# Kernel tuning notes

Measured on AMD Instinct MI355X. Metric: run time of the kernel, lower is better.

The kernel has to match this reference:

```python
import jax, jax.numpy as jnp
import numpy as np

LN_EPS = 1e-5
NEG_INF = -1e30


def setup_inputs() -> dict:
    key = jax.random.key(0)
    k1, k2, k3 = jax.random.split(key, 3)
    B, N, D = 8192, 64, 64
    fi = jax.random.normal(k1, (B, N, D), dtype=jnp.float32)
    # orthogonal-init correlation matrix (matches nn.init.orthogonal_)
    a = jax.random.normal(k2, (D, D), dtype=jnp.float32)
    q, r = jnp.linalg.qr(a)
    correlation_mat = q * jnp.sign(jnp.diag(r))[None, :]
    ln1_gamma = jnp.ones((D,), dtype=jnp.float32)
    ln1_beta = jnp.zeros((D,), dtype=jnp.float32)
    last_w = jax.random.normal(k3, (1, 2 * D), dtype=jnp.float32) * 0.05
    last_b = jnp.zeros((1,), dtype=jnp.float32)
    return {"fi": fi, "correlation_mat": correlation_mat,
            "ln1_gamma": ln1_gamma, "ln1_beta": ln1_beta,
            "last_w": last_w, "last_b": last_b}


def _layer_norm(x, gamma, beta):
    mu = jnp.mean(x, axis=-1, keepdims=True)
    var = jnp.mean(jnp.square(x - mu), axis=-1, keepdims=True)
    return (x - mu) * jax.lax.rsqrt(var + LN_EPS) * gamma + beta


def reference(fi, correlation_mat, ln1_gamma, ln1_beta, last_w, last_b):
    B, N, D = fi.shape
    # pairwise bilinear scores: beta[b,i,j] = fi[b,i] @ C @ fi[b,j]
    fiC = jnp.einsum('bid,de->bie', fi, correlation_mat)        # [B,N,D]
    beta = jnp.einsum('bie,bje->bij', fiC, fi)                  # [B,N,N]
    # exclude self (i==j), matching the Python loop which skips j==i
    diag_mask = jnp.eye(N, dtype=bool)
    beta = jnp.where(diag_mask[None, :, :], NEG_INF, beta)
    alpha = jax.nn.softmax(beta, axis=-1)                       # [B,N,N]
    vi = jnp.einsum('bij,bjd->bid', alpha, fi)                  # [B,N,D]
    vi = jax.nn.relu(_layer_norm(vi, ln1_gamma, ln1_beta))
    all_inputs = jnp.concatenate([fi, vi], axis=-1)             # [B,N,2D]
    weight = jax.nn.sigmoid(jnp.einsum('bnk,ok->bno', all_inputs, last_w) + last_b)
    return weight  # [B, N, 1]
```

## Files before the change

kernel.cpp:

```cpp
#include <hip/hip_runtime.h>
#include <hip/hip_bf16.h>

typedef __attribute__((ext_vector_type(8))) short short8;
typedef __attribute__((ext_vector_type(4))) float floatx4;

constexpr float LN_EPS = 1e-5f;
constexpr float NEG_INF_V = -1e30f;

__device__ __forceinline__ unsigned short bf16hi_sw(float x) {
    unsigned int u = __builtin_bit_cast(unsigned int, x);
    u += 0x7FFFu + ((u >> 16) & 1u);
    return (unsigned short)(u >> 16);
}
__device__ __forceinline__ float bf16f(unsigned short h) {
    unsigned int u = ((unsigned int)h) << 16;
    return __builtin_bit_cast(float, u);
}
__device__ __forceinline__ unsigned int pk2(float a, float b) {
    float2 f2; f2.x = a; f2.y = b;
    __hip_bfloat162 h2 = __float22bfloat162_rn(f2);
    unsigned int u;
    __builtin_memcpy(&u, &h2, sizeof(u));
    return u;
}
__device__ __forceinline__ void splitpk(float a, float b,
                                        unsigned int& H, unsigned int& L) {
    H = pk2(a, b);
    const float ha = __builtin_bit_cast(float, H << 16);
    const float hb = __builtin_bit_cast(float, H & 0xFFFF0000u);
    L = pk2(a - ha, b - hb);
}

__device__ __forceinline__ unsigned int permlo(unsigned int A, unsigned int B) {
    return __builtin_amdgcn_perm(B, A, 0x05040100u);
}
__device__ __forceinline__ unsigned int permhi(unsigned int A, unsigned int B) {
    return __builtin_amdgcn_perm(B, A, 0x07060302u);
}

template<int CTRL>
__device__ __forceinline__ float dppadd(float v) {
    int t = __builtin_amdgcn_update_dpp(0, __builtin_bit_cast(int, v),
                                        CTRL, 0xF, 0xF, true);
    return v + __builtin_bit_cast(float, t);
}
template<int CTRL>
__device__ __forceinline__ float dppmax(float v) {
    int t = __builtin_amdgcn_update_dpp(0, __builtin_bit_cast(int, v),
                                        CTRL, 0xF, 0xF, true);
    return fmaxf(v, __builtin_bit_cast(float, t));
}
__device__ __forceinline__ float rsum16(float v) {
    v = dppadd<0x121>(v); v = dppadd<0x122>(v);
    v = dppadd<0x124>(v); v = dppadd<0x128>(v);
    return v;
}
__device__ __forceinline__ float rmax16(float v) {
    v = dppmax<0x121>(v); v = dppmax<0x122>(v);
    v = dppmax<0x124>(v); v = dppmax<0x128>(v);
    return v;
}

__device__ __forceinline__ int eoff(int r, int c) {
    return r * 64 + ((((c >> 3) ^ r) & 7) << 3) + (c & 7);
}
__device__ __forceinline__ int goff(int r, int g) {
    return r * 64 + (((g ^ r) & 7) << 3);
}

__global__ void prep_corr(const float* __restrict__ corr,
                          unsigned short* __restrict__ ws) {
    const int tid  = threadIdx.x;
    const int lane = tid & 63;
    const int t    = tid >> 6;
    const int nn   = lane & 15;
    const int q    = lane >> 4;
    const int brow = 16 * t + nn;
    #pragma unroll
    for (int kk = 0; kk < 2; ++kk) {
        const int kbase = (kk * 4 + q) * 8;
        short8 H8, L8;
        #pragma unroll
        for (int e = 0; e < 8; ++e) {
            const float v = corr[(kbase + e) * 64 + brow];
            const unsigned short hh = bf16hi_sw(v);
            const unsigned short ll = bf16hi_sw(v - bf16f(hh));
            H8[e] = (short)hh;
            L8[e] = (short)ll;
        }
        const int idx = ((t * 2 + kk) * 64 + lane) * 8;
        *(short8*)&ws[idx]        = H8;
        *(short8*)&ws[4096 + idx] = L8;
    }
}

template<bool USEWS>
__global__ __launch_bounds__(256, 4)
void attn_mfma(const float* __restrict__ fi,
               const float* __restrict__ corr,
               const unsigned short* __restrict__ wsC,
               const float* __restrict__ ln_g,
               const float* __restrict__ ln_b,
               const float* __restrict__ lw,
               const float* __restrict__ lb,
               float* __restrict__ out)
{
    __shared__ __align__(16) unsigned short sFiH[4096], sFiL[4096];
    __shared__ __align__(16) unsigned short sFtH[4096];
    __shared__ __align__(16) unsigned short sPH[4096], sPL[4096];

    const int tid  = threadIdx.x;
    const int lane = tid & 63;
    const int w    = tid >> 6;
    const int n    = lane & 15;
    const int quad = lane >> 4;
    const size_t blk = blockIdx.x;

    const short8* wCH = (const short8*)wsC;
    const short8* wCL = (const short8*)(wsC + 4096);

    const int C = 4 * n;
    const int R = 4 * (tid >> 4);
    float d0v[4];
    {
        const float* fb = fi + blk * 4096;
        float4 v[4];
        #pragma unroll
        for (int i = 0; i < 4; ++i)
            v[i] = *(const float4*)(fb + (R + i) * 64 + C);

        const float4 w0v = *(const float4*)&lw[C];
        #pragma unroll
        for (int i = 0; i < 4; ++i) {
            float p = v[i].x * w0v.x + v[i].y * w0v.y
                    + v[i].z * w0v.z + v[i].w * w0v.w;
            d0v[i] = rsum16(p);
        }

        unsigned int H01[4], H23[4], L01[4], L23[4];
        #pragma unroll
        for (int i = 0; i < 4; ++i) {
            splitpk(v[i].x, v[i].y, H01[i], L01[i]);
            splitpk(v[i].z, v[i].w, H23[i], L23[i]);
        }
        #pragma unroll
        for (int i = 0; i < 4; ++i) {
            uint2 H = {H01[i], H23[i]};
            uint2 L = {L01[i], L23[i]};
            *(uint2*)&sFiH[eoff(R + i, C)] = H;
            *(uint2*)&sFiL[eoff(R + i, C)] = L;
        }
        uint2 t0 = {permlo(H01[0], H01[1]), permlo(H01[2], H01[3])};
        uint2 t1 = {permhi(H01[0], H01[1]), permhi(H01[2], H01[3])};
        uint2 t2 = {permlo(H23[0], H23[1]), permlo(H23[2], H23[3])};
        uint2 t3 = {permhi(H23[0], H23[1]), permhi(H23[2], H23[3])};
        *(uint2*)&sFtH[eoff(C + 0, R)] = t0;
        *(uint2*)&sFtH[eoff(C + 1, R)] = t1;
        *(uint2*)&sFtH[eoff(C + 2, R)] = t2;
        *(uint2*)&sFtH[eoff(C + 3, R)] = t3;
    }

    if constexpr (!USEWS) {
        float4 cv[4];
        #pragma unroll
        for (int i = 0; i < 4; ++i)
            cv[i] = *(const float4*)(corr + (size_t)(R + i) * 64 + C);
        unsigned int cH01[4], cH23[4], cL01[4], cL23[4];
        #pragma unroll
        for (int i = 0; i < 4; ++i) {
            splitpk(cv[i].x, cv[i].y, cH01[i], cL01[i]);
            splitpk(cv[i].z, cv[i].w, cH23[i], cL23[i]);
        }
        uint2 h0 = {permlo(cH01[0], cH01[1]), permlo(cH01[2], cH01[3])};
        uint2 h1 = {permhi(cH01[0], cH01[1]), permhi(cH01[2], cH01[3])};
        uint2 h2 = {permlo(cH23[0], cH23[1]), permlo(cH23[2], cH23[3])};
        uint2 h3 = {permhi(cH23[0], cH23[1]), permhi(cH23[2], cH23[3])};
        uint2 l0 = {permlo(cL01[0], cL01[1]), permlo(cL01[2], cL01[3])};
        uint2 l1 = {permhi(cL01[0], cL01[1]), permhi(cL01[2], cL01[3])};
        uint2 l2 = {permlo(cL23[0], cL23[1]), permlo(cL23[2], cL23[3])};
        uint2 l3 = {permhi(cL23[0], cL23[1]), permhi(cL23[2], cL23[3])};
        *(uint2*)&sPH[eoff(C + 0, R)] = h0;  *(uint2*)&sPL[eoff(C + 0, R)] = l0;
        *(uint2*)&sPH[eoff(C + 1, R)] = h1;  *(uint2*)&sPL[eoff(C + 1, R)] = l1;
        *(uint2*)&sPH[eoff(C + 2, R)] = h2;  *(uint2*)&sPL[eoff(C + 2, R)] = l2;
        *(uint2*)&sPH[eoff(C + 3, R)] = h3;  *(uint2*)&sPL[eoff(C + 3, R)] = l3;
        __syncthreads();
    }

    const int arow = 16 * w + n;

    short8 Ah[2], Al[2];
    #pragma unroll
    for (int kk = 0; kk < 2; ++kk) {
        Ah[kk] = *(const short8*)&sFiH[goff(arow, kk * 4 + quad)];
        Al[kk] = *(const short8*)&sFiL[goff(arow, kk * 4 + quad)];
    }
    floatx4 acc1[4];
    #pragma unroll
    for (int t = 0; t < 4; ++t) {
        floatx4 acc = {0.f, 0.f, 0.f, 0.f};
        #pragma unroll
        for (int kk = 0; kk < 2; ++kk) {
            short8 bh, bl;
            if constexpr (USEWS) {
                const int f = t * 2 + kk;
                bh = wCH[f * 64 + lane];
                bl = wCL[f * 64 + lane];
            } else {
                const int brow = 16 * t + n;
                bh = *(const short8*)&sPH[goff(brow, kk * 4 + quad)];
                bl = *(const short8*)&sPL[goff(brow, kk * 4 + quad)];
            }
            acc = __builtin_amdgcn_mfma_f32_16x16x32_bf16(Ah[kk], bh, acc, 0, 0, 0);
            acc = __builtin_amdgcn_mfma_f32_16x16x32_bf16(Al[kk], bh, acc, 0, 0, 0);
            acc = __builtin_amdgcn_mfma_f32_16x16x32_bf16(Ah[kk], bl, acc, 0, 0, 0);
        }
        acc1[t] = acc;
    }

    if constexpr (!USEWS) __syncthreads();

    #pragma unroll
    for (int t = 0; t < 4; ++t) {
        const int col = 16 * t + n;
        const int row = 16 * w + quad * 4;
        unsigned int H01, L01, H23, L23;
        splitpk(acc1[t][0], acc1[t][1], H01, L01);
        splitpk(acc1[t][2], acc1[t][3], H23, L23);
        sPH[eoff(row + 0, col)] = (unsigned short)H01;
        sPH[eoff(row + 1, col)] = (unsigned short)(H01 >> 16);
        sPH[eoff(row + 2, col)] = (unsigned short)H23;
        sPH[eoff(row + 3, col)] = (unsigned short)(H23 >> 16);
        sPL[eoff(row + 0, col)] = (unsigned short)L01;
        sPL[eoff(row + 1, col)] = (unsigned short)(L01 >> 16);
        sPL[eoff(row + 2, col)] = (unsigned short)L23;
        sPL[eoff(row + 3, col)] = (unsigned short)(L23 >> 16);
    }

    if constexpr (USEWS) __syncthreads();

    short8 PAh[2], PAl[2];
    #pragma unroll
    for (int kk = 0; kk < 2; ++kk) {
        PAh[kk] = *(const short8*)&sPH[goff(arow, kk * 4 + quad)];
        PAl[kk] = *(const short8*)&sPL[goff(arow, kk * 4 + quad)];
    }
    floatx4 acc2[4];
    #pragma unroll
    for (int t = 0; t < 4; ++t) {
        floatx4 acc = {0.f, 0.f, 0.f, 0.f};
        const int brow = 16 * t + n;
        #pragma unroll
        for (int kk = 0; kk < 2; ++kk) {
            short8 bh = *(const short8*)&sFiH[goff(brow, kk * 4 + quad)];
            short8 bl = *(const short8*)&sFiL[goff(brow, kk * 4 + quad)];
            acc = __builtin_amdgcn_mfma_f32_16x16x32_bf16(PAh[kk], bh, acc, 0, 0, 0);
            acc = __builtin_amdgcn_mfma_f32_16x16x32_bf16(PAl[kk], bh, acc, 0, 0, 0);
            acc = __builtin_amdgcn_mfma_f32_16x16x32_bf16(PAh[kk], bl, acc, 0, 0, 0);
        }
        acc2[t] = acc;
    }

    #pragma unroll
    for (int reg = 0; reg < 4; ++reg) {
        const int row = 16 * w + quad * 4 + reg;
        float x[4];
        #pragma unroll
        for (int t = 0; t < 4; ++t) {
            x[t] = acc2[t][reg];
            if (row == 16 * t + n) x[t] = NEG_INF_V;
        }
        float m = fmaxf(fmaxf(x[0], x[1]), fmaxf(x[2], x[3]));
        m = rmax16(m);
        #pragma unroll
        for (int t = 0; t < 4; ++t) x[t] = __expf(x[t] - m);
        const unsigned int A01 = pk2(x[0], x[1]);
        const unsigned int A23 = pk2(x[2], x[3]);
        sPH[eoff(row, 0 + n)]  = (unsigned short)A01;
        sPH[eoff(row, 16 + n)] = (unsigned short)(A01 >> 16);
        sPH[eoff(row, 32 + n)] = (unsigned short)A23;
        sPH[eoff(row, 48 + n)] = (unsigned short)(A23 >> 16);
    }

    short8 AAh[2];
    #pragma unroll
    for (int kk = 0; kk < 2; ++kk)
        AAh[kk] = *(const short8*)&sPH[goff(arow, kk * 4 + quad)];
    floatx4 acc3[4];
    #pragma unroll
    for (int t = 0; t < 4; ++t) {
        floatx4 acc = {0.f, 0.f, 0.f, 0.f};
        const int brow = 16 * t + n;
        #pragma unroll
        for (int kk = 0; kk < 2; ++kk) {
            short8 bh = *(const short8*)&sFtH[goff(brow, kk * 4 + quad)];
            acc = __builtin_amdgcn_mfma_f32_16x16x32_bf16(AAh[kk], bh, acc, 0, 0, 0);
        }
        acc3[t] = acc;
    }

    float gv[4], bv[4], w1v[4];
    #pragma unroll
    for (int t = 0; t < 4; ++t) {
        gv[t]  = ln_g[16 * t + n];
        bv[t]  = ln_b[16 * t + n];
        w1v[t] = lw[64 + 16 * t + n];
    }
    const float bias = lb[0];
    float res[4];
    #pragma unroll
    for (int reg = 0; reg < 4; ++reg) {
        float s  = acc3[0][reg] + acc3[1][reg] + acc3[2][reg] + acc3[3][reg];
        float s2 = acc3[0][reg] * acc3[0][reg] + acc3[1][reg] * acc3[1][reg]
                 + acc3[2][reg] * acc3[2][reg] + acc3[3][reg] * acc3[3][reg];
        s  = rsum16(s);
        s2 = rsum16(s2);
        const float mu  = s * (1.0f / 64.0f);
        const float var = s2 * (1.0f / 64.0f) - mu * mu;
        const float rstd = __builtin_amdgcn_rsqf(var + LN_EPS);
        float dotp = 0.f;
        #pragma unroll
        for (int t = 0; t < 4; ++t) {
            float lnv = (acc3[t][reg] - mu) * rstd * gv[t] + bv[t];
            lnv = fmaxf(lnv, 0.f);
            dotp += lnv * w1v[t];
        }
        dotp = rsum16(dotp);
        res[reg] = __builtin_amdgcn_rcpf(1.0f + __expf(-(dotp + d0v[reg] + bias)));
    }
    if (n == 0) {
        float4 o = {res[0], res[1], res[2], res[3]};
        *(float4*)&out[blk * 64 + 16 * w + quad * 4] = o;
    }
}

extern "C" void kernel_launch(void* const* d_in, const int* in_sizes, int n_in,
                              void* d_out, int out_size, void* d_ws, size_t ws_size,
                              hipStream_t stream) {
    const float* fi   = (const float*)d_in[0];
    const float* corr = (const float*)d_in[1];
    const float* g    = (const float*)d_in[2];
    const float* b    = (const float*)d_in[3];
    const float* lw   = (const float*)d_in[4];
    const float* lb   = (const float*)d_in[5];
    float* out        = (float*)d_out;

    const int B = in_sizes[0] / 4096;

    if (d_ws != nullptr && ws_size >= 16384) {
        unsigned short* wsC = (unsigned short*)d_ws;
        hipLaunchKernelGGL(prep_corr, dim3(1), dim3(256), 0, stream, corr, wsC);
        hipLaunchKernelGGL(HIP_KERNEL_NAME(attn_mfma<true>), dim3(B), dim3(256), 0,
                           stream, fi, corr, wsC, g, b, lw, lb, out);
    } else {
        hipLaunchKernelGGL(HIP_KERNEL_NAME(attn_mfma<false>), dim3(B), dim3(256), 0,
                           stream, fi, corr, (const unsigned short*)nullptr,
                           g, b, lw, lb, out);
    }
}
```

Baseline: 214.6 us.

## Use per-wave scratch for fiC tiles and shrink LDS to raise occupancy

Swaps the two block-wide 8 KB P buffers (hi/lo) for one 8 KB scratch region split per wave. Each wave stages only its own fiC rows, in two K-halves, plus its own softmax rows, so the barrier between the fiC write and the score MMA is no longer needed. The lower LDS use lets launch bounds rise from 4 to 5 blocks per CU. The split correlation matrix moves from the workspace argument to a device global array, and the fallback path without a workspace is removed.

After: 214.8 us. No clear change (+0.1%).

```diff
diff --git a/kernel.cpp b/kernel.cpp
--- a/kernel.cpp
+++ b/kernel.cpp
@@ -6,6 +6,8 @@
 
 constexpr float LN_EPS = 1e-5f;
 constexpr float NEG_INF_V = -1e30f;
+
+__device__ unsigned short g_wsC[8192];
 
 __device__ __forceinline__ unsigned short bf16hi_sw(float x) {
     unsigned int u = __builtin_bit_cast(unsigned int, x);
@@ -67,9 +69,14 @@
 __device__ __forceinline__ int goff(int r, int g) {
     return r * 64 + (((g ^ r) & 7) << 3);
 }
-
-__global__ void prep_corr(const float* __restrict__ corr,
-                          unsigned short* __restrict__ ws) {
+__device__ __forceinline__ int moff(int r, int c) {
+    return r * 32 + ((((c >> 3) ^ (r >> 2)) & 3) << 3) + (c & 7);
+}
+__device__ __forceinline__ int aoff(int r, int c) {
+    return r * 64 + ((((c >> 3) ^ (r >> 2)) & 7) << 3) + (c & 7);
+}
+
+__global__ void prep_corr(const float* __restrict__ corr) {
     const int tid  = threadIdx.x;
     const int lane = tid & 63;
     const int t    = tid >> 6;
@@ -89,16 +96,13 @@
             L8[e] = (short)ll;
         }
         const int idx = ((t * 2 + kk) * 64 + lane) * 8;
-        *(short8*)&ws[idx]        = H8;
-        *(short8*)&ws[4096 + idx] = L8;
-    }
-}
-
-template<bool USEWS>
-__global__ __launch_bounds__(256, 4)
+        *(short8*)&g_wsC[idx]        = H8;
+        *(short8*)&g_wsC[4096 + idx] = L8;
+    }
+}
+
+__global__ __launch_bounds__(256, 5)
 void attn_mfma(const float* __restrict__ fi,
-               const float* __restrict__ corr,
-               const unsigned short* __restrict__ wsC,
                const float* __restrict__ ln_g,
                const float* __restrict__ ln_b,
                const float* __restrict__ lw,
@@ -107,7 +111,7 @@
 {
     __shared__ __align__(16) unsigned short sFiH[4096], sFiL[4096];
     __shared__ __align__(16) unsigned short sFtH[4096];
-    __shared__ __align__(16) unsigned short sPH[4096], sPL[4096];
+    __shared__ __align__(16) unsigned short sM[4096];
 
     const int tid  = threadIdx.x;
     const int lane = tid & 63;
@@ -116,8 +120,10 @@
     const int quad = lane >> 4;
     const size_t blk = blockIdx.x;
 
-    const short8* wCH = (const short8*)wsC;
-    const short8* wCL = (const short8*)(wsC + 4096);
+    unsigned short* mW = &sM[w * 1024];
+
+    const short8* wCH = (const short8*)g_wsC;
+    const short8* wCL = (const short8*)(g_wsC + 4096);
 
     const int C = 4 * n;
     const int R = 4 * (tid >> 4);
@@ -160,32 +166,6 @@
         *(uint2*)&sFtH[eoff(C + 3, R)] = t3;
     }
 
-    if constexpr (!USEWS) {
-        float4 cv[4];
-        #pragma unroll
-        for (int i = 0; i < 4; ++i)
-            cv[i] = *(const float4*)(corr + (size_t)(R + i) * 64 + C);
-        unsigned int cH01[4], cH23[4], cL01[4], cL23[4];
-        #pragma unroll
-        for (int i = 0; i < 4; ++i) {
-            splitpk(cv[i].x, cv[i].y, cH01[i], cL01[i]);
-            splitpk(cv[i].z, cv[i].w, cH23[i], cL23[i]);
-        }
-        uint2 h0 = {permlo(cH01[0], cH01[1]), permlo(cH01[2], cH01[3])};
-        uint2 h1 = {permhi(cH01[0], cH01[1]), permhi(cH01[2], cH01[3])};
-        uint2 h2 = {permlo(cH23[0], cH23[1]), permlo(cH23[2], cH23[3])};
-        uint2 h3 = {permhi(cH23[0], cH23[1]), permhi(cH23[2], cH23[3])};
-        uint2 l0 = {permlo(cL01[0], cL01[1]), permlo(cL01[2], cL01[3])};
-        uint2 l1 = {permhi(cL01[0], cL01[1]), permhi(cL01[2], cL01[3])};
-        uint2 l2 = {permlo(cL23[0], cL23[1]), permlo(cL23[2], cL23[3])};
-        uint2 l3 = {permhi(cL23[0], cL23[1]), permhi(cL23[2], cL23[3])};
-        *(uint2*)&sPH[eoff(C + 0, R)] = h0;  *(uint2*)&sPL[eoff(C + 0, R)] = l0;
-        *(uint2*)&sPH[eoff(C + 1, R)] = h1;  *(uint2*)&sPL[eoff(C + 1, R)] = l1;
-        *(uint2*)&sPH[eoff(C + 2, R)] = h2;  *(uint2*)&sPL[eoff(C + 2, R)] = l2;
-        *(uint2*)&sPH[eoff(C + 3, R)] = h3;  *(uint2*)&sPL[eoff(C + 3, R)] = l3;
-        __syncthreads();
-    }
-
     const int arow = 16 * w + n;
 
     short8 Ah[2], Al[2];
@@ -200,16 +180,9 @@
         floatx4 acc = {0.f, 0.f, 0.f, 0.f};
         #pragma unroll
         for (int kk = 0; kk < 2; ++kk) {
-            short8 bh, bl;
-            if constexpr (USEWS) {
-                const int f = t * 2 + kk;
-                bh = wCH[f * 64 + lane];
-                bl = wCL[f * 64 + lane];
-            } else {
-                const int brow = 16 * t + n;
-                bh = *(const short8*)&sPH[goff(brow, kk * 4 + quad)];
-                bl = *(const short8*)&sPL[goff(brow, kk * 4 + quad)];
-            }
+            const int f = t * 2 + kk;
+            short8 bh = wCH[f * 64 + lane];
+            short8 bl = wCL[f * 64 + lane];
             acc = __builtin_amdgcn_mfma_f32_16x16x32_bf16(Ah[kk], bh, acc, 0, 0, 0);
             acc = __builtin_amdgcn_mfma_f32_16x16x32_bf16(Al[kk], bh, acc, 0, 0, 0);
             acc = __builtin_amdgcn_mfma_f32_16x16x32_bf16(Ah[kk], bl, acc, 0, 0, 0);
@@ -217,47 +190,42 @@
         acc1[t] = acc;
     }
 
-    if constexpr (!USEWS) __syncthreads();
-
-    #pragma unroll
-    for (int t = 0; t < 4; ++t) {
-        const int col = 16 * t + n;
-        const int row = 16 * w + quad * 4;
-        unsigned int H01, L01, H23, L23;
-        splitpk(acc1[t][0], acc1[t][1], H01, L01);
-        splitpk(acc1[t][2], acc1[t][3], H23, L23);
-        sPH[eoff(row + 0, col)] = (unsigned short)H01;
-        sPH[eoff(row + 1, col)] = (unsigned short)(H01 >> 16);
-        sPH[eoff(row + 2, col)] = (unsigned short)H23;
-        sPH[eoff(row + 3, col)] = (unsigned short)(H23 >> 16);
-        sPL[eoff(row + 0, col)] = (unsigned short)L01;
-        sPL[eoff(row + 1, col)] = (unsigned short)(L01 >> 16);
-        sPL[eoff(row + 2, col)] = (unsigned short)L23;
-        sPL[eoff(row + 3, col)] = (unsigned short)(L23 >> 16);
-    }
-
-    if constexpr (USEWS) __syncthreads();
-
-    short8 PAh[2], PAl[2];
-    #pragma unroll
-    for (int kk = 0; kk < 2; ++kk) {
-        PAh[kk] = *(const short8*)&sPH[goff(arow, kk * 4 + quad)];
-        PAl[kk] = *(const short8*)&sPL[goff(arow, kk * 4 + quad)];
-    }
+    __syncthreads();
+
     floatx4 acc2[4];
     #pragma unroll
-    for (int t = 0; t < 4; ++t) {
-        floatx4 acc = {0.f, 0.f, 0.f, 0.f};
-        const int brow = 16 * t + n;
-        #pragma unroll
-        for (int kk = 0; kk < 2; ++kk) {
-            short8 bh = *(const short8*)&sFiH[goff(brow, kk * 4 + quad)];
-            short8 bl = *(const short8*)&sFiL[goff(brow, kk * 4 + quad)];
-            acc = __builtin_amdgcn_mfma_f32_16x16x32_bf16(PAh[kk], bh, acc, 0, 0, 0);
-            acc = __builtin_amdgcn_mfma_f32_16x16x32_bf16(PAl[kk], bh, acc, 0, 0, 0);
-            acc = __builtin_amdgcn_mfma_f32_16x16x32_bf16(PAh[kk], bl, acc, 0, 0, 0);
-        }
-        acc2[t] = acc;
+    for (int t = 0; t < 4; ++t) acc2[t] = floatx4{0.f, 0.f, 0.f, 0.f};
+
+    #pragma unroll
+    for (int kh = 0; kh < 2; ++kh) {
+        #pragma unroll
+        for (int th = 0; th < 2; ++th) {
+            const int t = 2 * kh + th;
+            unsigned int H01, L01, H23, L23;
+            splitpk(acc1[t][0], acc1[t][1], H01, L01);
+            splitpk(acc1[t][2], acc1[t][3], H23, L23);
+            const int c  = 16 * th + n;
+            const int r0 = 4 * quad;
+            mW[moff(r0 + 0, c)]       = (unsigned short)H01;
+            mW[moff(r0 + 1, c)]       = (unsigned short)(H01 >> 16);
+            mW[moff(r0 + 2, c)]       = (unsigned short)H23;
+            mW[moff(r0 + 3, c)]       = (unsigned short)(H23 >> 16);
+            mW[512 + moff(r0 + 0, c)] = (unsigned short)L01;
+            mW[512 + moff(r0 + 1, c)] = (unsigned short)(L01 >> 16);
+            mW[512 + moff(r0 + 2, c)] = (unsigned short)L23;
+            mW[512 + moff(r0 + 3, c)] = (unsigned short)(L23 >> 16);
+        }
+        short8 PAh = *(const short8*)&mW[moff(n, quad * 8)];
+        short8 PAl = *(const short8*)&mW[512 + moff(n, quad * 8)];
+        #pragma unroll
+        for (int t = 0; t < 4; ++t) {
+            const int brow = 16 * t + n;
+            short8 bh = *(const short8*)&sFiH[goff(brow, kh * 4 + quad)];
+            short8 bl = *(const short8*)&sFiL[goff(brow, kh * 4 + quad)];
+            acc2[t] = __builtin_amdgcn_mfma_f32_16x16x32_bf16(PAh, bh, acc2[t], 0, 0, 0);
+            acc2[t] = __builtin_amdgcn_mfma_f32_16x16x32_bf16(PAl, bh, acc2[t], 0, 0, 0);
+            acc2[t] = __builtin_amdgcn_mfma_f32_16x16x32_bf16(PAh, bl, acc2[t], 0, 0, 0);
+        }
     }
 
     #pragma unroll
@@ -275,16 +243,17 @@
         for (int t = 0; t < 4; ++t) x[t] = __expf(x[t] - m);
         const unsigned int A01 = pk2(x[0], x[1]);
         const unsigned int A23 = pk2(x[2], x[3]);
-        sPH[eoff(row, 0 + n)]  = (unsigned short)A01;
-        sPH[eoff(row, 16 + n)] = (unsigned short)(A01 >> 16);
-        sPH[eoff(row, 32 + n)] = (unsigned short)A23;
-        sPH[eoff(row, 48 + n)] = (unsigned short)(A23 >> 16);
+        const int lr = quad * 4 + reg;
+        mW[aoff(lr, 0 + n)]  = (unsigned short)A01;
+        mW[aoff(lr, 16 + n)] = (unsigned short)(A01 >> 16);
+        mW[aoff(lr, 32 + n)] = (unsigned short)A23;
+        mW[aoff(lr, 48 + n)] = (unsigned short)(A23 >> 16);
     }
 
     short8 AAh[2];
     #pragma unroll
     for (int kk = 0; kk < 2; ++kk)
-        AAh[kk] = *(const short8*)&sPH[goff(arow, kk * 4 + quad)];
+        AAh[kk] = *(const short8*)&mW[aoff(n, (kk * 4 + quad) * 8)];
     floatx4 acc3[4];
     #pragma unroll
     for (int t = 0; t < 4; ++t) {
@@ -345,15 +314,7 @@
     float* out        = (float*)d_out;
 
     const int B = in_sizes[0] / 4096;
-
-    if (d_ws != nullptr && ws_size >= 16384) {
-        unsigned short* wsC = (unsigned short*)d_ws;
-        hipLaunchKernelGGL(prep_corr, dim3(1), dim3(256), 0, stream, corr, wsC);
-        hipLaunchKernelGGL(HIP_KERNEL_NAME(attn_mfma<true>), dim3(B), dim3(256), 0,
-                           stream, fi, corr, wsC, g, b, lw, lb, out);
-    } else {
-        hipLaunchKernelGGL(HIP_KERNEL_NAME(attn_mfma<false>), dim3(B), dim3(256), 0,
-                           stream, fi, corr, (const unsigned short*)nullptr,
-                           g, b, lw, lb, out);
-    }
-}
+    hipLaunchKernelGGL(prep_corr, dim3(1), dim3(256), 0, stream, corr);
+    hipLaunchKernelGGL(attn_mfma, dim3(B), dim3(256), 0, stream,
+                       fi, g, b, lw, lb, out);
+}
```
